# Performance work log

Measured on AMD Instinct MI355X. Metric: run time of the kernel, lower is better.

## Reference

```python
import jax, jax.numpy as jnp
import numpy as np

# pool sizes (must match init_kwargs)
N_FQK, N_FV, N_REL, N_VAL, N_KNOW = 512, 256, 128, 32, 256
K_FQK, K_FV, K_REL, K_VAL = 64, 32, 16, 3
D_MODEL, D_SPACE = 1024, 64
B, S = 8, 2048


def _topk_sparsify(w, k):
    # keep top-k entries per row, zero the rest (values unchanged)
    vals, idx = jax.lax.top_k(w, k)                      # [B,k]
    out = jnp.zeros_like(w)
    rows = jnp.arange(w.shape[0])[:, None]
    return out.at[rows, idx].set(vals), idx


def setup_inputs() -> dict:
    key = jax.random.key(0)
    k1, k2, k3, k4 = jax.random.split(key, 4)
    x = jax.random.normal(k1, (B, S, D_MODEL), dtype=jnp.float32)
    # importance: per-token weights normalized over sequence
    importance = jax.nn.softmax(jax.random.normal(k2, (B, S), dtype=jnp.float32), axis=-1)
    W = jax.random.normal(k3, (D_MODEL, D_SPACE), dtype=jnp.float32) * 0.02
    b = jnp.zeros((D_SPACE,), dtype=jnp.float32)
    total = N_FQK + N_FV + N_REL + N_VAL + N_KNOW
    neuron_emb = jax.random.normal(k4, (total, D_SPACE), dtype=jnp.float32) * 0.02
    return {"x": x, "importance": importance, "W": W, "b": b, "neuron_emb": neuron_emb}


def reference(x, importance, W, b, neuron_emb):
    # projection (dropout inactive in eval); normalized neuron embeddings
    h = x @ W + b                                         # [B,S,d_space]
    emb_n = neuron_emb / jnp.linalg.norm(neuron_emb, axis=-1, keepdims=True)
    all_logits = jnp.einsum('bsd,nd->bsn', h, emb_n)      # [B,S,N_total]

    e0 = N_FQK
    e1 = e0 + N_FV
    e2 = e1 + N_REL
    e3 = e2 + N_VAL

    def route(lo, hi):
        pref = jax.nn.softmax(all_logits[..., lo:hi], axis=-1)  # [B,S,n]
        w = jnp.einsum('bs,bsn->bn', importance, pref)          # [B,n]
        return pref, w

    _, w_qk = route(0, e0)
    _, idx_qk = jax.lax.top_k(w_qk, K_FQK)
    idx_qk = jnp.sort(idx_qk, axis=-1)

    _, w_v = route(e0, e1)
    _, idx_v = jax.lax.top_k(w_v, K_FV)
    idx_v = jnp.sort(idx_v, axis=-1)

    # relational Q and K share the same logit slice (eval: no excitability bonus)
    _, w_rQ = route(e1, e2)
    _, w_rK = route(e1, e2)
    rw_Q, _ = _topk_sparsify(w_rQ, K_REL)
    rw_K, _ = _topk_sparsify(w_rK, K_REL)

    _, w_val = route(e2, e3)
    vw, _ = _topk_sparsify(w_val, K_VAL)

    return idx_qk, idx_v, rw_Q, rw_K, vw, w_qk, w_v
```

## Files before the change

### kernel.cpp

```cpp
#include <hip/hip_runtime.h>
#include <hip/hip_bf16.h>
#include <hip/hip_fp16.h>
#include <math.h>

#define ROWS  16384
#define DM    1024
#define DS    64
#define NUSE  928
#define NPAD  960
#define NT    15

typedef __attribute__((ext_vector_type(8))) short bf16x8;
typedef __attribute__((ext_vector_type(4))) float f32x4;

static __device__ inline f32x4 mfma16(bf16x8 a, bf16x8 b, f32x4 c) {
    return __builtin_amdgcn_mfma_f32_16x16x32_bf16(a, b, c, 0, 0, 0);
}

static __device__ inline void bfsplit(float v, unsigned short& h, unsigned short& l) {
    unsigned u = __float_as_uint(v);
    unsigned hr = u + 0x7FFFu + ((u >> 16) & 1u);
    h = (unsigned short)(hr >> 16);
    float hf = __uint_as_float((unsigned)h << 16);
    float r = v - hf;
    unsigned ur = __float_as_uint(r);
    unsigned lr2 = ur + 0x7FFFu + ((ur >> 16) & 1u);
    l = (unsigned short)(lr2 >> 16);
}

#define OFF_EBH  0LL
#define OFF_EBL  122880LL
#define OFF_WBH  245760LL
#define OFF_WBL  376832LL
#define OFF_HP   507904LL
#define OFF_WP   17285120LL

__global__ __launch_bounds__(256) void k_prep(const float* __restrict__ emb,
                                              const float* __restrict__ W,
                                              unsigned short* __restrict__ ebh,
                                              unsigned short* __restrict__ ebl,
                                              unsigned short* __restrict__ wbh,
                                              unsigned short* __restrict__ wbl) {
    if (blockIdx.x < 4) {
        int n = blockIdx.x * 256 + threadIdx.x;
        if (n >= NPAD) return;
        if (n >= NUSE) {
            #pragma unroll
            for (int d = 0; d < DS; d++) {
                int kt = d >> 5, q = (d >> 3) & 3, j = d & 7;
                int a = ((kt * 4 + q) * NPAD + n) * 8 + j;
                ebh[a] = 0; ebl[a] = 0;
            }
            return;
        }
        float ss = 0.f;
        #pragma unroll
        for (int d = 0; d < DS; d++) { float v = emb[n * DS + d]; ss = fmaf(v, v, ss); }
        float inv = 1.0f / sqrtf(ss);
        #pragma unroll
        for (int d = 0; d < DS; d++) {
            float v = emb[n * DS + d] * inv;
            unsigned short h, l; bfsplit(v, h, l);
            int kt = d >> 5, q = (d >> 3) & 3, j = d & 7;
            int a = ((kt * 4 + q) * NPAD + n) * 8 + j;
            ebh[a] = h; ebl[a] = l;
        }
    } else {
        int idx = (blockIdx.x - 4) * 256 + threadIdx.x;
        int ktg = idx >> 6, n = idx & 63;
        #pragma unroll
        for (int q = 0; q < 4; q++) {
            #pragma unroll
            for (int j = 0; j < 8; j++) {
                int k = ktg * 32 + q * 8 + j;
                float v = W[k * DS + n];
                unsigned short h, l; bfsplit(v, h, l);
                int a = ((ktg * 4 + q) * 64 + n) * 8 + j;
                wbh[a] = h; wbl[a] = l;
            }
        }
    }
}

__global__ __launch_bounds__(256, 4) void k_hmm(const float* __restrict__ x,
                                                const unsigned short* __restrict__ wbh,
                                                const unsigned short* __restrict__ wbl,
                                                float* __restrict__ hpart) {
    __shared__ unsigned short Ah[4 * 4 * 64 * 8];
    __shared__ unsigned short Al[4 * 4 * 64 * 8];
    const int tid = threadIdx.x;
    const int rc = blockIdx.x, g = blockIdx.y;
    const long long row0 = (long long)rc * 64;

    const int sr = tid >> 2, scg = tid & 3;
    const float* xrow = &x[(row0 + sr) * DM + g * 256 + scg * 32];

    const int w = tid >> 6, lane = tid & 63, q = lane >> 4, lm = lane & 15;
    f32x4 acc[4];
    #pragma unroll
    for (int f = 0; f < 4; f++) { acc[f].x = 0.f; acc[f].y = 0.f; acc[f].z = 0.f; acc[f].w = 0.f; }

    float4 pf[8];
    #pragma unroll
    for (int u = 0; u < 8; u++) pf[u] = *(const float4*)&xrow[u * 4];
    #pragma unroll
    for (int u = 0; u < 8; u++) {
        int qq = u >> 1, j0 = (u & 1) * 4;
        int base = ((scg * 4 + qq) * 64 + sr) * 8 + j0;
        unsigned short h0, l0, h1, l1, h2, l2, h3, l3;
        bfsplit(pf[u].x, h0, l0); bfsplit(pf[u].y, h1, l1);
        bfsplit(pf[u].z, h2, l2); bfsplit(pf[u].w, h3, l3);
        uint2 ph; ph.x = (unsigned)h0 | ((unsigned)h1 << 16); ph.y = (unsigned)h2 | ((unsigned)h3 << 16);
        uint2 pl; pl.x = (unsigned)l0 | ((unsigned)l1 << 16); pl.y = (unsigned)l2 | ((unsigned)l3 << 16);
        *(uint2*)&Ah[base] = ph;
        *(uint2*)&Al[base] = pl;
    }
    __syncthreads();

    #pragma unroll
    for (int u = 0; u < 8; u++) pf[u] = *(const float4*)&xrow[128 + u * 4];

    #pragma unroll
    for (int kt = 0; kt < 4; kt++) {
        const bf16x8 a_h = *(const bf16x8*)&Ah[((kt * 4 + q) * 64 + w * 16 + lm) * 8];
        const bf16x8 a_l = *(const bf16x8*)&Al[((kt * 4 + q) * 64 + w * 16 + lm) * 8];
        const int ktg = g * 8 + kt;
        #pragma unroll
        for (int f = 0; f < 4; f++) {
            int ba = ((ktg * 4 + q) * 64 + f * 16 + lm) * 8;
            bf16x8 b_h = *(const bf16x8*)&wbh[ba];
            bf16x8 b_l = *(const bf16x8*)&wbl[ba];
            acc[f] = mfma16(a_h, b_h, acc[f]);
            acc[f] = mfma16(a_h, b_l, acc[f]);
            acc[f] = mfma16(a_l, b_h, acc[f]);
        }
    }
    __syncthreads();

    #pragma unroll
    for (int u = 0; u < 8; u++) {
        int qq = u >> 1, j0 = (u & 1) * 4;
        int base = ((scg * 4 + qq) * 64 + sr) * 8 + j0;
        unsigned short h0, l0, h1, l1, h2, l2, h3, l3;
        bfsplit(pf[u].x, h0, l0); bfsplit(pf[u].y, h1, l1);
        bfsplit(pf[u].z, h2, l2); bfsplit(pf[u].w, h3, l3);
        uint2 ph; ph.x = (unsigned)h0 | ((unsigned)h1 << 16); ph.y = (unsigned)h2 | ((unsigned)h3 << 16);
        uint2 pl; pl.x = (unsigned)l0 | ((unsigned)l1 << 16); pl.y = (unsigned)l2 | ((unsigned)l3 << 16);
        *(uint2*)&Ah[base] = ph;
        *(uint2*)&Al[base] = pl;
    }
    __syncthreads();

    #pragma unroll
    for (int kt = 0; kt < 4; kt++) {
        const bf16x8 a_h = *(const bf16x8*)&Ah[((kt * 4 + q) * 64 + w * 16 + lm) * 8];
        const bf16x8 a_l = *(const bf16x8*)&Al[((kt * 4 + q) * 64 + w * 16 + lm) * 8];
        const int ktg = g * 8 + 4 + kt;
        #pragma unroll
        for (int f = 0; f < 4; f++) {
            int ba = ((ktg * 4 + q) * 64 + f * 16 + lm) * 8;
            bf16x8 b_h = *(const bf16x8*)&wbh[ba];
            bf16x8 b_l = *(const bf16x8*)&wbl[ba];
            acc[f] = mfma16(a_h, b_h, acc[f]);
            acc[f] = mfma16(a_h, b_l, acc[f]);
            acc[f] = mfma16(a_l, b_h, acc[f]);
        }
    }

    float* hp = &hpart[((long long)g * ROWS + row0) * 64];
    #pragma unroll
    for (int f = 0; f < 4; f++) {
        #pragma unroll
        for (int t = 0; t < 4; t++) {
            hp[(w * 16 + q * 4 + t) * 64 + f * 16 + lm] = acc[f][t];
        }
    }
}

__global__ __launch_bounds__(1024, 4) void k_zpw(const float* __restrict__ hpart,
                                                 const float* __restrict__ bias,
                                                 const unsigned short* __restrict__ ebh,
                                                 const unsigned short* __restrict__ ebl,
                                                 const float* __restrict__ imp,
                                                 float* __restrict__ wpart) {
    __shared__ __align__(16) unsigned short Ph[NPAD * 72];
    __shared__ __align__(16) unsigned short Ah[2 * 4 * 64 * 8];
    __shared__ __align__(16) unsigned short Al[2 * 4 * 64 * 8];
    __shared__ float zslot[4][4][64];
    __shared__ float coefL[64 * 4];

    const int tid = threadIdx.x;
    const int rc = blockIdx.x;

    if (tid < 1024) ((float*)zslot)[tid] = 0.f;

    {
        int r = tid >> 4, seg = tid & 15;
        int col = seg * 4;
        float4 s = *(const float4*)&bias[col];
        #pragma unroll
        for (int g = 0; g < 4; g++) {
            float4 a = *(const float4*)&hpart[((long long)g * ROWS + rc * 64 + r) * 64 + col];
            s.x += a.x; s.y += a.y; s.z += a.z; s.w += a.w;
        }
        unsigned short h0, l0, h1, l1, h2, l2, h3, l3;
        bfsplit(s.x, h0, l0); bfsplit(s.y, h1, l1);
        bfsplit(s.z, h2, l2); bfsplit(s.w, h3, l3);
        int kt = seg >> 3, q = (seg >> 1) & 3, j0 = (seg & 1) * 4;
        int base = ((kt * 4 + q) * 64 + r) * 8 + j0;
        uint2 ph; ph.x = (unsigned)h0 | ((unsigned)h1 << 16); ph.y = (unsigned)h2 | ((unsigned)h3 << 16);
        uint2 pl; pl.x = (unsigned)l0 | ((unsigned)l1 << 16); pl.y = (unsigned)l2 | ((unsigned)l3 << 16);
        *(uint2*)&Ah[base] = ph;
        *(uint2*)&Al[base] = pl;
    }
    __syncthreads();

    const int w = tid >> 6, lane = tid & 63, q = lane >> 4, lm = lane & 15;
    const int rw = w & 3, wg = w >> 2;

    bf16x8 a_h[2], a_l[2];
    #pragma unroll
    for (int kt = 0; kt < 2; kt++) {
        int ab = ((kt * 4 + q) * 64 + rw * 16 + lm) * 8;
        a_h[kt] = *(const bf16x8*)&Ah[ab];
        a_l[kt] = *(const bf16x8*)&Al[ab];
    }

    #pragma unroll
    for (int v = 0; v < 4; v++) {
        int nt = wg + v * 4;
        if (nt > 14) continue;
        f32x4 acc[4];
        #pragma unroll
        for (int f = 0; f < 4; f++) { acc[f].x = 0.f; acc[f].y = 0.f; acc[f].z = 0.f; acc[f].w = 0.f; }
        #pragma unroll
        for (int kt = 0; kt < 2; kt++) {
            #pragma unroll
            for (int f = 0; f < 4; f++) {
                int bb = ((kt * 4 + q) * NPAD + nt * 64 + f * 16 + lm) * 8;
                bf16x8 b_h = *(const bf16x8*)&ebh[bb];
                bf16x8 b_l = *(const bf16x8*)&ebl[bb];
                acc[f] = mfma16(a_h[kt], b_h, acc[f]);
                acc[f] = mfma16(a_h[kt], b_l, acc[f]);
                acc[f] = mfma16(a_l[kt], b_h, acc[f]);
            }
        }
        const int sl = (nt < 8) ? 0 : (nt < 12) ? 1 : (nt < 14) ? 2 : 3;
        float s0 = 0.f, s1 = 0.f, s2 = 0.f, s3 = 0.f;
        #pragma unroll
        for (int f = 0; f < 4; f++) {
            float e0 = __expf(acc[f][0]);
            float e1 = __expf(acc[f][1]);
            float e2 = __expf(acc[f][2]);
            float e3 = __expf(acc[f][3]);
            int n = nt * 64 + f * 16 + lm;
            unsigned short p0 = __half_as_ushort(__float2half(e0));
            unsigned short p1 = __half_as_ushort(__float2half(e1));
            unsigned short p2 = __half_as_ushort(__float2half(e2));
            unsigned short p3 = __half_as_ushort(__float2half(e3));
            uint2 pk; pk.x = (unsigned)p0 | ((unsigned)p1 << 16); pk.y = (unsigned)p2 | ((unsigned)p3 << 16);
            *(uint2*)&Ph[n * 72 + rw * 16 + q * 4] = pk;
            if (nt * 64 + f * 16 < NUSE) {
                s0 += e0; s1 += e1; s2 += e2; s3 += e3;
            }
        }
        #pragma unroll
        for (int off = 1; off < 16; off <<= 1) {
            s0 += __shfl_xor(s0, off); s1 += __shfl_xor(s1, off);
            s2 += __shfl_xor(s2, off); s3 += __shfl_xor(s3, off);
        }
        if (lm < 4) {
            float sv = (lm == 0) ? s0 : (lm == 1) ? s1 : (lm == 2) ? s2 : s3;
            zslot[wg][sl][rw * 16 + q * 4 + lm] += sv;
        }
    }
    __syncthreads();

    if (tid < 64) {
        int r = tid;
        float im = imp[rc * 64 + r];
        #pragma unroll
        for (int sl = 0; sl < 4; sl++) {
            float Z = zslot[0][sl][r] + zslot[1][sl][r] + zslot[2][sl][r] + zslot[3][sl][r];
            coefL[r * 4 + sl] = im / Z;
        }
    }
    __syncthreads();

    if (tid < NUSE) {
        int n = tid;
        int sl = (n < 512) ? 0 : (n < 768) ? 1 : (n < 896) ? 2 : 3;
        float acc = 0.f;
        #pragma unroll
        for (int rb = 0; rb < 8; rb++) {
            uint4 pk = *(const uint4*)&Ph[n * 72 + rb * 8];
            const unsigned pv[4] = {pk.x, pk.y, pk.z, pk.w};
            #pragma unroll
            for (int u = 0; u < 4; u++) {
                float v0 = __half2float(__ushort_as_half((unsigned short)(pv[u] & 0xFFFF)));
                float v1 = __half2float(__ushort_as_half((unsigned short)(pv[u] >> 16)));
                int row = rb * 8 + u * 2;
                acc = fmaf(coefL[(row + 0) * 4 + sl], v0, acc);
                acc = fmaf(coefL[(row + 1) * 4 + sl], v1, acc);
            }
        }
        wpart[(long long)rc * NPAD + n] = acc;
    }
}

__global__ __launch_bounds__(512) void k_out(const float* __restrict__ wpart,
                                             float* __restrict__ out) {
    const int b = blockIdx.x;
    const int tid = threadIdx.x;
    __shared__ float w_s[NUSE];
    __shared__ int   rk[NUSE];

    for (int n = tid; n < NUSE; n += 512) {
        float s = 0.f;
        #pragma unroll 4
        for (int c = 0; c < 32; c++)
            s += wpart[(long long)(b * 32 + c) * NPAD + n];
        w_s[n] = s;
        if (n < 512)      out[3072 + (long long)b * 512 + n] = s;
        else if (n < 768) out[7168 + (long long)b * 256 + (n - 512)] = s;
    }
    __syncthreads();

    for (int n = tid; n < NUSE; n += 512) {
        int lo, hi;
        if (n < 512)      { lo = 0;   hi = 512; }
        else if (n < 768) { lo = 512; hi = 768; }
        else if (n < 896) { lo = 768; hi = 896; }
        else              { lo = 896; hi = NUSE; }
        float wn = w_s[n];
        int r = 0;
        for (int m = lo; m < hi; m++) {
            float wm = w_s[m];
            r += (wm > wn) || ((wm == wn) && (m < n));
        }
        rk[n] = r;
    }
    __syncthreads();

    if (tid < 512) {
        int n = tid;
        if (rk[n] < 64) {
            int pos = 0;
            for (int m = 0; m < n; m++) pos += (rk[m] < 64) ? 1 : 0;
            out[(long long)b * 64 + pos] = (float)n;
        }
    }
    if (tid < 256) {
        int n = 512 + tid;
        if (rk[n] < 32) {
            int pos = 0;
            for (int m = 512; m < n; m++) pos += (rk[m] < 32) ? 1 : 0;
            out[512 + (long long)b * 32 + pos] = (float)tid;
        }
    }
    if (tid < 128) {
        int n = 768 + tid;
        float v = (rk[n] < 16) ? w_s[n] : 0.f;
        out[768 + (long long)b * 128 + tid] = v;
        out[1792 + (long long)b * 128 + tid] = v;
    }
    if (tid < 32) {
        int n = 896 + tid;
        float v = (rk[n] < 3) ? w_s[n] : 0.f;
        out[2816 + (long long)b * 32 + tid] = v;
    }
}

extern "C" void kernel_launch(void* const* d_in, const int* in_sizes, int n_in,
                              void* d_out, int out_size, void* d_ws, size_t ws_size,
                              hipStream_t stream) {
    const float* x    = (const float*)d_in[0];
    const float* imp  = (const float*)d_in[1];
    const float* W    = (const float*)d_in[2];
    const float* bias = (const float*)d_in[3];
    const float* emb  = (const float*)d_in[4];

    char* ws = (char*)d_ws;
    unsigned short* ebh = (unsigned short*)(ws + OFF_EBH);
    unsigned short* ebl = (unsigned short*)(ws + OFF_EBL);
    unsigned short* wbh = (unsigned short*)(ws + OFF_WBH);
    unsigned short* wbl = (unsigned short*)(ws + OFF_WBL);
    float* hpart        = (float*)(ws + OFF_HP);
    float* wpart        = (float*)(ws + OFF_WP);
    float* out          = (float*)d_out;

    k_prep<<<12, 256, 0, stream>>>(emb, W, ebh, ebl, wbh, wbl);
    k_hmm<<<dim3(256, 4), 256, 0, stream>>>(x, wbh, wbl, hpart);
    k_zpw<<<256, 1024, 0, stream>>>(hpart, bias, ebh, ebl, imp, wpart);
    k_out<<<8, 512, 0, stream>>>(wpart, out);
}
```

Before: 167.0 us.

## Fuse x@W projection into the logits/softmax kernel, dropping the hpart round-trip

```diff
diff --git a/kernel.cpp b/kernel.cpp
--- a/kernel.cpp
+++ b/kernel.cpp
@@ -32,8 +32,7 @@
 #define OFF_EBL  122880LL
 #define OFF_WBH  245760LL
 #define OFF_WBL  376832LL
-#define OFF_HP   507904LL
-#define OFF_WP   17285120LL
+#define OFF_WP   507904LL
 
 __global__ __launch_bounds__(256) void k_prep(const float* __restrict__ emb,
                                               const float* __restrict__ W,
@@ -82,148 +81,103 @@
     }
 }
 
-__global__ __launch_bounds__(256, 4) void k_hmm(const float* __restrict__ x,
-                                                const unsigned short* __restrict__ wbh,
-                                                const unsigned short* __restrict__ wbl,
-                                                float* __restrict__ hpart) {
-    __shared__ unsigned short Ah[4 * 4 * 64 * 8];
-    __shared__ unsigned short Al[4 * 4 * 64 * 8];
-    const int tid = threadIdx.x;
-    const int rc = blockIdx.x, g = blockIdx.y;
-    const long long row0 = (long long)rc * 64;
-
-    const int sr = tid >> 2, scg = tid & 3;
-    const float* xrow = &x[(row0 + sr) * DM + g * 256 + scg * 32];
-
-    const int w = tid >> 6, lane = tid & 63, q = lane >> 4, lm = lane & 15;
-    f32x4 acc[4];
-    #pragma unroll
-    for (int f = 0; f < 4; f++) { acc[f].x = 0.f; acc[f].y = 0.f; acc[f].z = 0.f; acc[f].w = 0.f; }
-
-    float4 pf[8];
-    #pragma unroll
-    for (int u = 0; u < 8; u++) pf[u] = *(const float4*)&xrow[u * 4];
-    #pragma unroll
-    for (int u = 0; u < 8; u++) {
-        int qq = u >> 1, j0 = (u & 1) * 4;
-        int base = ((scg * 4 + qq) * 64 + sr) * 8 + j0;
-        unsigned short h0, l0, h1, l1, h2, l2, h3, l3;
-        bfsplit(pf[u].x, h0, l0); bfsplit(pf[u].y, h1, l1);
-        bfsplit(pf[u].z, h2, l2); bfsplit(pf[u].w, h3, l3);
-        uint2 ph; ph.x = (unsigned)h0 | ((unsigned)h1 << 16); ph.y = (unsigned)h2 | ((unsigned)h3 << 16);
-        uint2 pl; pl.x = (unsigned)l0 | ((unsigned)l1 << 16); pl.y = (unsigned)l2 | ((unsigned)l3 << 16);
-        *(uint2*)&Ah[base] = ph;
-        *(uint2*)&Al[base] = pl;
-    }
-    __syncthreads();
-
-    #pragma unroll
-    for (int u = 0; u < 8; u++) pf[u] = *(const float4*)&xrow[128 + u * 4];
-
-    #pragma unroll
-    for (int kt = 0; kt < 4; kt++) {
-        const bf16x8 a_h = *(const bf16x8*)&Ah[((kt * 4 + q) * 64 + w * 16 + lm) * 8];
-        const bf16x8 a_l = *(const bf16x8*)&Al[((kt * 4 + q) * 64 + w * 16 + lm) * 8];
-        const int ktg = g * 8 + kt;
-        #pragma unroll
-        for (int f = 0; f < 4; f++) {
-            int ba = ((ktg * 4 + q) * 64 + f * 16 + lm) * 8;
-            bf16x8 b_h = *(const bf16x8*)&wbh[ba];
-            bf16x8 b_l = *(const bf16x8*)&wbl[ba];
-            acc[f] = mfma16(a_h, b_h, acc[f]);
-            acc[f] = mfma16(a_h, b_l, acc[f]);
-            acc[f] = mfma16(a_l, b_h, acc[f]);
-        }
-    }
-    __syncthreads();
-
-    #pragma unroll
-    for (int u = 0; u < 8; u++) {
-        int qq = u >> 1, j0 = (u & 1) * 4;
-        int base = ((scg * 4 + qq) * 64 + sr) * 8 + j0;
-        unsigned short h0, l0, h1, l1, h2, l2, h3, l3;
-        bfsplit(pf[u].x, h0, l0); bfsplit(pf[u].y, h1, l1);
-        bfsplit(pf[u].z, h2, l2); bfsplit(pf[u].w, h3, l3);
-        uint2 ph; ph.x = (unsigned)h0 | ((unsigned)h1 << 16); ph.y = (unsigned)h2 | ((unsigned)h3 << 16);
-        uint2 pl; pl.x = (unsigned)l0 | ((unsigned)l1 << 16); pl.y = (unsigned)l2 | ((unsigned)l3 << 16);
-        *(uint2*)&Ah[base] = ph;
-        *(uint2*)&Al[base] = pl;
-    }
-    __syncthreads();
-
-    #pragma unroll
-    for (int kt = 0; kt < 4; kt++) {
-        const bf16x8 a_h = *(const bf16x8*)&Ah[((kt * 4 + q) * 64 + w * 16 + lm) * 8];
-        const bf16x8 a_l = *(const bf16x8*)&Al[((kt * 4 + q) * 64 + w * 16 + lm) * 8];
-        const int ktg = g * 8 + 4 + kt;
-        #pragma unroll
-        for (int f = 0; f < 4; f++) {
-            int ba = ((ktg * 4 + q) * 64 + f * 16 + lm) * 8;
-            bf16x8 b_h = *(const bf16x8*)&wbh[ba];
-            bf16x8 b_l = *(const bf16x8*)&wbl[ba];
-            acc[f] = mfma16(a_h, b_h, acc[f]);
-            acc[f] = mfma16(a_h, b_l, acc[f]);
-            acc[f] = mfma16(a_l, b_h, acc[f]);
-        }
-    }
-
-    float* hp = &hpart[((long long)g * ROWS + row0) * 64];
-    #pragma unroll
-    for (int f = 0; f < 4; f++) {
-        #pragma unroll
-        for (int t = 0; t < 4; t++) {
-            hp[(w * 16 + q * 4 + t) * 64 + f * 16 + lm] = acc[f][t];
-        }
-    }
-}
-
-__global__ __launch_bounds__(1024, 4) void k_zpw(const float* __restrict__ hpart,
-                                                 const float* __restrict__ bias,
-                                                 const unsigned short* __restrict__ ebh,
-                                                 const unsigned short* __restrict__ ebl,
-                                                 const float* __restrict__ imp,
-                                                 float* __restrict__ wpart) {
-    __shared__ __align__(16) unsigned short Ph[NPAD * 72];
-    __shared__ __align__(16) unsigned short Ah[2 * 4 * 64 * 8];
-    __shared__ __align__(16) unsigned short Al[2 * 4 * 64 * 8];
-    __shared__ float zslot[4][4][64];
-    __shared__ float coefL[64 * 4];
+__global__ __launch_bounds__(1024, 4) void k_mega(const float* __restrict__ x,
+                                                  const float* __restrict__ bias,
+                                                  const unsigned short* __restrict__ wbh,
+                                                  const unsigned short* __restrict__ wbl,
+                                                  const unsigned short* __restrict__ ebh,
+                                                  const unsigned short* __restrict__ ebl,
+                                                  const float* __restrict__ imp,
+                                                  float* __restrict__ wpart) {
+    __shared__ __align__(16) unsigned char smem[159744];
+    unsigned short* Ph = (unsigned short*)smem;
+    unsigned short* Xh = (unsigned short*)smem;
+    unsigned short* Xl = (unsigned short*)(smem + 16384);
+    unsigned short* Hh = (unsigned short*)(smem + 138240);
+    unsigned short* Hl = (unsigned short*)(smem + 146432);
+    float* zslot = (float*)(smem + 154624);
+    float* coefL = (float*)(smem + 158720);
 
     const int tid = threadIdx.x;
     const int rc = blockIdx.x;
-
-    if (tid < 1024) ((float*)zslot)[tid] = 0.f;
+    const long long row0 = (long long)rc * 64;
+
+    zslot[tid & 1023] = 0.f;
+
+    const int w = tid >> 6, lane = tid & 63, q = lane >> 4, lm = lane & 15;
+
+    const int rg = w >> 2, cg = w & 3;
+    const int sr = tid >> 4, ss = tid & 15;
+    const float* xrow = &x[(row0 + sr) * DM + ss * 8];
+    const int skt = ss >> 2, sq = ss & 3;
+    const int sbase = ((skt * 4 + sq) * 64 + sr) * 8;
+
+    f32x4 hacc;
+    hacc.x = 0.f; hacc.y = 0.f; hacc.z = 0.f; hacc.w = 0.f;
+
+    float4 pf0 = *(const float4*)&xrow[0];
+    float4 pf1 = *(const float4*)&xrow[4];
+
+    for (int ch = 0; ch < 8; ch++) {
+        if (ch) __syncthreads();
+        {
+            unsigned short h0, l0, h1, l1, h2, l2, h3, l3;
+            bfsplit(pf0.x, h0, l0); bfsplit(pf0.y, h1, l1);
+            bfsplit(pf0.z, h2, l2); bfsplit(pf0.w, h3, l3);
+            uint2 ph; ph.x = (unsigned)h0 | ((unsigned)h1 << 16); ph.y = (unsigned)h2 | ((unsigned)h3 << 16);
+            uint2 pl; pl.x = (unsigned)l0 | ((unsigned)l1 << 16); pl.y = (unsigned)l2 | ((unsigned)l3 << 16);
+            *(uint2*)&Xh[sbase] = ph;
+            *(uint2*)&Xl[sbase] = pl;
+            bfsplit(pf1.x, h0, l0); bfsplit(pf1.y, h1, l1);
+            bfsplit(pf1.z, h2, l2); bfsplit(pf1.w, h3, l3);
+            ph.x = (unsigned)h0 | ((unsigned)h1 << 16); ph.y = (unsigned)h2 | ((unsigned)h3 << 16);
+            pl.x = (unsigned)l0 | ((unsigned)l1 << 16); pl.y = (unsigned)l2 | ((unsigned)l3 << 16);
+            *(uint2*)&Xh[sbase + 4] = ph;
+            *(uint2*)&Xl[sbase + 4] = pl;
+        }
+        if (ch < 7) {
+            pf0 = *(const float4*)&xrow[(ch + 1) * 128];
+            pf1 = *(const float4*)&xrow[(ch + 1) * 128 + 4];
+        }
+        __syncthreads();
+        #pragma unroll
+        for (int kt = 0; kt < 4; kt++) {
+            const bf16x8 a_h = *(const bf16x8*)&Xh[((kt * 4 + q) * 64 + rg * 16 + lm) * 8];
+            const bf16x8 a_l = *(const bf16x8*)&Xl[((kt * 4 + q) * 64 + rg * 16 + lm) * 8];
+            const int ktg = ch * 4 + kt;
+            const int ba = ((ktg * 4 + q) * 64 + cg * 16 + lm) * 8;
+            const bf16x8 b_h = *(const bf16x8*)&wbh[ba];
+            const bf16x8 b_l = *(const bf16x8*)&wbl[ba];
+            hacc = mfma16(a_h, b_h, hacc);
+            hacc = mfma16(a_h, b_l, hacc);
+            hacc = mfma16(a_l, b_h, hacc);
+        }
+    }
+    __syncthreads();
 
     {
-        int r = tid >> 4, seg = tid & 15;
-        int col = seg * 4;
-        float4 s = *(const float4*)&bias[col];
-        #pragma unroll
-        for (int g = 0; g < 4; g++) {
-            float4 a = *(const float4*)&hpart[((long long)g * ROWS + rc * 64 + r) * 64 + col];
-            s.x += a.x; s.y += a.y; s.z += a.z; s.w += a.w;
-        }
-        unsigned short h0, l0, h1, l1, h2, l2, h3, l3;
-        bfsplit(s.x, h0, l0); bfsplit(s.y, h1, l1);
-        bfsplit(s.z, h2, l2); bfsplit(s.w, h3, l3);
-        int kt = seg >> 3, q = (seg >> 1) & 3, j0 = (seg & 1) * 4;
-        int base = ((kt * 4 + q) * 64 + r) * 8 + j0;
-        uint2 ph; ph.x = (unsigned)h0 | ((unsigned)h1 << 16); ph.y = (unsigned)h2 | ((unsigned)h3 << 16);
-        uint2 pl; pl.x = (unsigned)l0 | ((unsigned)l1 << 16); pl.y = (unsigned)l2 | ((unsigned)l3 << 16);
-        *(uint2*)&Ah[base] = ph;
-        *(uint2*)&Al[base] = pl;
-    }
-    __syncthreads();
-
-    const int w = tid >> 6, lane = tid & 63, q = lane >> 4, lm = lane & 15;
+        const int D = cg * 16 + lm;
+        const float bv = bias[D];
+        const int ktD = D >> 5, qD = (D >> 3) & 3, jD = D & 7;
+        #pragma unroll
+        for (int t = 0; t < 4; t++) {
+            const int R = rg * 16 + q * 4 + t;
+            float v = hacc[t] + bv;
+            unsigned short hh, ll; bfsplit(v, hh, ll);
+            Hh[((ktD * 4 + qD) * 64 + R) * 8 + jD] = hh;
+            Hl[((ktD * 4 + qD) * 64 + R) * 8 + jD] = ll;
+        }
+    }
+    __syncthreads();
+
     const int rw = w & 3, wg = w >> 2;
 
     bf16x8 a_h[2], a_l[2];
     #pragma unroll
     for (int kt = 0; kt < 2; kt++) {
         int ab = ((kt * 4 + q) * 64 + rw * 16 + lm) * 8;
-        a_h[kt] = *(const bf16x8*)&Ah[ab];
-        a_l[kt] = *(const bf16x8*)&Al[ab];
+        a_h[kt] = *(const bf16x8*)&Hh[ab];
+        a_l[kt] = *(const bf16x8*)&Hl[ab];
     }
 
     #pragma unroll
@@ -271,7 +225,7 @@
         }
         if (lm < 4) {
             float sv = (lm == 0) ? s0 : (lm == 1) ? s1 : (lm == 2) ? s2 : s3;
-            zslot[wg][sl][rw * 16 + q * 4 + lm] += sv;
+            zslot[(wg * 4 + sl) * 64 + rw * 16 + q * 4 + lm] += sv;
         }
     }
     __syncthreads();
@@ -281,7 +235,8 @@
         float im = imp[rc * 64 + r];
         #pragma unroll
         for (int sl = 0; sl < 4; sl++) {
-            float Z = zslot[0][sl][r] + zslot[1][sl][r] + zslot[2][sl][r] + zslot[3][sl][r];
+            float Z = zslot[(0 * 4 + sl) * 64 + r] + zslot[(1 * 4 + sl) * 64 + r]
+                    + zslot[(2 * 4 + sl) * 64 + r] + zslot[(3 * 4 + sl) * 64 + r];
             coefL[r * 4 + sl] = im / Z;
         }
     }
@@ -385,12 +340,10 @@
     unsigned short* ebl = (unsigned short*)(ws + OFF_EBL);
     unsigned short* wbh = (unsigned short*)(ws + OFF_WBH);
     unsigned short* wbl = (unsigned short*)(ws + OFF_WBL);
-    float* hpart        = (float*)(ws + OFF_HP);
     float* wpart        = (float*)(ws + OFF_WP);
     float* out          = (float*)d_out;
 
     k_prep<<<12, 256, 0, stream>>>(emb, W, ebh, ebl, wbh, wbl);
-    k_hmm<<<dim3(256, 4), 256, 0, stream>>>(x, wbh, wbl, hpart);
-    k_zpw<<<256, 1024, 0, stream>>>(hpart, bias, ebh, ebl, imp, wpart);
+    k_mega<<<256, 1024, 0, stream>>>(x, bias, wbh, wbl, ebh, ebl, imp, wpart);
     k_out<<<8, 512, 0, stream>>>(wpart, out);
 }
```

Result: faster. 158.6 us (-5.0%).
